# Optimization experiments

Hardware: AMD Instinct MI355X
Metric: run time of the kernel (lower is better)

## Reference

```python
import jax, jax.numpy as jnp
import numpy as np

N = 50000        # num_nodes
D = 512          # input_dim == output_dim (residual update requires equality)
EU = 100000      # undirected edges; directed E = 2*EU = 200000
STEP = 0.5       # step_size


def setup_inputs() -> dict:
    key = jax.random.key(0)
    ks = jax.random.split(key, 5)
    x = jax.random.normal(ks[0], (N, D), jnp.float32)
    # symmetric edge list without self loops: store (s,d) then (d,s)
    src = jax.random.randint(ks[1], (EU,), 0, N, dtype=jnp.int32)
    off = jax.random.randint(ks[2], (EU,), 1, N, dtype=jnp.int32)
    dst = (src + off) % N
    edge_index = jnp.stack([jnp.concatenate([src, dst]),
                            jnp.concatenate([dst, src])])  # [2, 2*EU]
    # reverse-edge index: edge e < EU reverses to e+EU and vice versa
    ar = jnp.arange(EU, dtype=jnp.int32)
    right_idx = jnp.concatenate([ar + EU, ar])
    # params: nn.Linear(D, D) and sheaf_learner nn.Linear(2D, 1, bias=False)
    W_lin = jax.random.normal(ks[3], (D, D), jnp.float32) / np.sqrt(D)
    b_lin = jnp.zeros((D,), jnp.float32)
    w_sheaf = jax.random.normal(ks[4], (2 * D,), jnp.float32) / np.sqrt(2 * D)
    return {"x": x, "W_lin": W_lin, "b_lin": b_lin, "w_sheaf": w_sheaf,
            "edge_index": edge_index, "right_idx": right_idx}


def reference(x, W_lin, b_lin, w_sheaf, edge_index, right_idx):
    row, col = edge_index[0], edge_index[1]
    d = x.shape[1]
    # sheaf_learner(cat([x_row, x_col])) == (x @ w[:d])[row] + (x @ w[d:])[col]
    s = x @ w_sheaf[:d]                      # [N]
    t = x @ w_sheaf[d:]                      # [N]
    maps = jnp.tanh(s[row] + t[col])         # [E] scalar restriction maps
    # off-diagonal Laplacian values: -F_e(row) * F_reverse(e)
    non_diag = -maps * maps[right_idx]       # [E]
    diag_maps = jax.ops.segment_sum(maps ** 2, row, num_segments=N)  # [N]
    d_inv = (diag_maps + 1.0) ** -0.5        # [N]
    norm_maps = d_inv[row] * non_diag * d_inv[col]                   # [E]
    diag = d_inv * diag_maps * d_inv                                 # [N]
    # y = linear(x); L @ y done as diag term + edge scatter
    y = x @ W_lin.T + b_lin                  # [N, D]
    Ly = diag[:, None] * y + jax.ops.segment_sum(
        norm_maps[:, None] * y[col], row, num_segments=N)
    return x - STEP * Ly
```

## Files before the change

### kernel.cpp

```cpp
#include <hip/hip_runtime.h>
#include <hip/hip_bf16.h>
#include <cstdint>
#include <cstddef>


#define DD 512
#define STEPSZ 0.5f
#define SLOTS 32

typedef __bf16 bf16;
typedef __bf16 bf16x8 __attribute__((ext_vector_type(8)));
typedef __bf16 bf16x4 __attribute__((ext_vector_type(4)));
typedef float f32x4 __attribute__((ext_vector_type(4)));

#define GLOAD16(g, l)                                                     \
  __builtin_amdgcn_global_load_lds(                                       \
      (const __attribute__((address_space(1))) void*)(g),                 \
      (__attribute__((address_space(3))) void*)(l), 16, 0, 0)

__global__ __launch_bounds__(256) void k_prep(
    const float* __restrict__ x, const float* __restrict__ wsheaf,
    const float* __restrict__ wlin, bf16* __restrict__ xbf,
    bf16* __restrict__ wbf, float* __restrict__ s, float* __restrict__ t,
    float* __restrict__ dmaps, int* __restrict__ fill, int n) {
  if (blockIdx.x < 256) {
    int i = (blockIdx.x * 256 + threadIdx.x) * 4;
    float4 v = *(const float4*)(wlin + i);
    bf16x4 p;
    p[0] = (bf16)v.x; p[1] = (bf16)v.y; p[2] = (bf16)v.z; p[3] = (bf16)v.w;
    *(bf16x4*)(wbf + i) = p;
    int zi = blockIdx.x * 256 + threadIdx.x;
    if (zi < n) { dmaps[zi] = 0.0f; fill[zi] = 0; }
    return;
  }
  int lane = threadIdx.x & 63;
  int row = ((blockIdx.x - 256) << 2) + (threadIdx.x >> 6);
  if (row >= n) return;
  const float* xr = x + (size_t)row * DD + lane * 8;
  float4 a = *(const float4*)xr;
  float4 b = *(const float4*)(xr + 4);
  bf16x8 p;
  p[0] = (bf16)a.x; p[1] = (bf16)a.y; p[2] = (bf16)a.z; p[3] = (bf16)a.w;
  p[4] = (bf16)b.x; p[5] = (bf16)b.y; p[6] = (bf16)b.z; p[7] = (bf16)b.w;
  *(bf16x8*)(xbf + (size_t)row * DD + lane * 8) = p;
  const float* w1 = wsheaf + lane * 8;
  const float* w2 = wsheaf + DD + lane * 8;
  float4 wa = *(const float4*)w1, wb = *(const float4*)(w1 + 4);
  float4 wc = *(const float4*)w2, wd = *(const float4*)(w2 + 4);
  float sv = a.x * wa.x + a.y * wa.y + a.z * wa.z + a.w * wa.w +
             b.x * wb.x + b.y * wb.y + b.z * wb.z + b.w * wb.w;
  float tv = a.x * wc.x + a.y * wc.y + a.z * wc.z + a.w * wc.w +
             b.x * wd.x + b.y * wd.y + b.z * wd.z + b.w * wd.w;
  #pragma unroll
  for (int o = 32; o > 0; o >>= 1) {
    sv += __shfl_xor(sv, o);
    tv += __shfl_xor(tv, o);
  }
  if (lane == 0) { s[row] = sv; t[row] = tv; }
}

__global__ __launch_bounds__(256) void k_fill(
    const int* __restrict__ ei, const float* __restrict__ s,
    const float* __restrict__ t, float* __restrict__ dmaps,
    int* __restrict__ fill, int* __restrict__ ccol, float* __restrict__ cval,
    int E) {
  int e = blockIdx.x * 256 + threadIdx.x;
  if (e >= E) return;
  int r = ei[e], c = ei[E + e];
  float sr = s[r], tc = t[c], sc = s[c], tr = t[r];
  float me = tanhf(sr + tc);
  float mr = tanhf(sc + tr);
  atomicAdd(dmaps + r, me * me);
  int p = atomicAdd(fill + r, 1);
  if (p < SLOTS) {
    ccol[(size_t)r * SLOTS + p] = c;
    cval[(size_t)r * SLOTS + p] = -me * mr;
  }
}

__global__ __launch_bounds__(256) void k_gather(
    const bf16* __restrict__ xb, const float* __restrict__ dmaps,
    const int* __restrict__ fill, const int* __restrict__ ccol,
    const float* __restrict__ cval, bf16* __restrict__ u,
    float* __restrict__ cb, int n) {
  int lane = threadIdx.x & 63;
  int row = (blockIdx.x << 2) + (threadIdx.x >> 6);
  if (row >= n) return;
  int c0 = lane * 8;
  float dm = dmaps[row];
  float inv_r = rsqrtf(dm + 1.0f);
  float dg = dm / (dm + 1.0f);
  bf16x8 xv = *(const bf16x8*)(xb + (size_t)row * DD + c0);
  float acc[8];
  #pragma unroll
  for (int j = 0; j < 8; ++j) acc[j] = dg * (float)xv[j];
  int cnt = fill[row];
  if (cnt > SLOTS) cnt = SLOTS;
  const int* cc = ccol + (size_t)row * SLOTS;
  const float* cv = cval + (size_t)row * SLOTS;
  unsigned nm1 = (unsigned)(n - 1);
  float cbs = 0.0f;
  for (int i = 0; i < cnt; i += 4) {
    int4 c4 = *(const int4*)(cc + i);
    float4 v4 = *(const float4*)(cv + i);
    int rem = cnt - i;
    unsigned ca = min((unsigned)c4.x, nm1);
    unsigned cbi = min((unsigned)c4.y, nm1);
    unsigned cg = min((unsigned)c4.z, nm1);
    unsigned cd = min((unsigned)c4.w, nm1);
    bf16x8 na = *(const bf16x8*)(xb + (size_t)ca * DD + c0);
    bf16x8 nb = *(const bf16x8*)(xb + (size_t)cbi * DD + c0);
    bf16x8 ng = *(const bf16x8*)(xb + (size_t)cg * DD + c0);
    bf16x8 nd = *(const bf16x8*)(xb + (size_t)cd * DD + c0);
    float va = rem > 0 ? v4.x * inv_r * rsqrtf(dmaps[ca] + 1.0f) : 0.0f;
    float vb = rem > 1 ? v4.y * inv_r * rsqrtf(dmaps[cbi] + 1.0f) : 0.0f;
    float vg = rem > 2 ? v4.z * inv_r * rsqrtf(dmaps[cg] + 1.0f) : 0.0f;
    float vd = rem > 3 ? v4.w * inv_r * rsqrtf(dmaps[cd] + 1.0f) : 0.0f;
    cbs += va + vb + vg + vd;
    #pragma unroll
    for (int j = 0; j < 8; ++j)
      acc[j] += va * (float)na[j] + vb * (float)nb[j] + vg * (float)ng[j] +
                vd * (float)nd[j];
  }
  bf16x8 o;
  #pragma unroll
  for (int j = 0; j < 8; ++j) o[j] = (bf16)acc[j];
  *(bf16x8*)(u + (size_t)row * DD + c0) = o;
  if (lane == 0) cb[row] = dg + cbs;
}

__global__ __launch_bounds__(256, 4) void k_gemm(
    const bf16* __restrict__ ub, const bf16* __restrict__ wbf,
    const float* __restrict__ bias, const float* __restrict__ x,
    const bf16* __restrict__ xb, const float* __restrict__ cb,
    float* __restrict__ out, int M, int nwg, int use_bf) {
  __shared__ __align__(16) char smem[36864];
  bf16* lds = (bf16*)smem;
  int orig = blockIdx.x;
  int q = nwg >> 3, r = nwg & 7;
  int xcd = orig & 7;
  int wgid = (xcd < r ? xcd * (q + 1) : r * (q + 1) + (xcd - r) * q) +
             (orig >> 3);
  int bm = wgid >> 2, bn = wgid & 3;
  int tid = threadIdx.x, w = tid >> 6, lane = tid & 63;
  int wr = w >> 1, wc = w & 1;
  int lhi = lane >> 4;

  int row_local = lane >> 2;
  int kc = (lane & 3) ^ (row_local & 3);
  const bf16* gA[2];
  const bf16* gB[2];
  bf16* lA[2];
  bf16* lB[2];
  #pragma unroll
  for (int c = 0; c < 2; ++c) {
    int rloc = c * 64 + w * 16 + row_local;
    int ga = bm * 128 + rloc;
    if (ga > M - 1) ga = M - 1;
    gA[c] = ub + (size_t)ga * DD + kc * 8;
    gB[c] = wbf + (size_t)(bn * 128 + rloc) * DD + kc * 8;
    lA[c] = lds + (c * 64 + w * 16) * 32;
    lB[c] = lds + 4096 + (c * 64 + w * 16) * 32;
  }

  f32x4 acc[4][4] = {};
  int arow = (wr * 64 + (lane & 15)) * 32;
  int brow = (wc * 64 + (lane & 15)) * 32;
  int sl = ((lhi ^ (lane & 3))) * 8;

  #pragma unroll
  for (int c = 0; c < 2; ++c) {
    GLOAD16(gA[c], lA[c]);
    GLOAD16(gB[c], lB[c]);
  }
  __syncthreads();

  #pragma unroll
  for (int t = 0; t < 16; ++t) {
    int cbuf = (t & 1) * 8192;
    if (t + 1 < 16) {
      int nbuf = ((t + 1) & 1) * 8192;
      int k0 = (t + 1) * 32;
      #pragma unroll
      for (int c = 0; c < 2; ++c) {
        GLOAD16(gA[c] + k0, lA[c] + nbuf);
        GLOAD16(gB[c] + k0, lB[c] + nbuf);
      }
    }
    const bf16* base = lds + cbuf;
    bf16x8 af[4], bfr[4];
    #pragma unroll
    for (int m = 0; m < 4; ++m)
      af[m] = *(const bf16x8*)(base + arow + m * 512 + sl);
    #pragma unroll
    for (int nn = 0; nn < 4; ++nn)
      bfr[nn] = *(const bf16x8*)(base + 4096 + brow + nn * 512 + sl);
    #pragma unroll
    for (int m = 0; m < 4; ++m)
      #pragma unroll
      for (int nn = 0; nn < 4; ++nn)
        acc[m][nn] = __builtin_amdgcn_mfma_f32_16x16x32_bf16(
            af[m], bfr[nn], acc[m][nn], 0, 0, 0);
    __syncthreads();
  }

  int rowbase = bm * 128 + wr * 64;
  int clamped = rowbase + lane;
  if (clamped > M - 1) clamped = M - 1;
  float cbl = cb[clamped];
  float* ltile = (float*)smem + w * 2304;
  int prow = lane >> 3;
  int pc4 = lane & 7;
  #pragma unroll
  for (int h = 0; h < 2; ++h) {
    #pragma unroll
    for (int m = 0; m < 4; ++m)
      #pragma unroll
      for (int n2 = 0; n2 < 2; ++n2)
        #pragma unroll
        for (int rr = 0; rr < 4; ++rr) {
          int row = m * 16 + lhi * 4 + rr;
          ltile[row * 36 + n2 * 16 + (lane & 15)] = acc[m][h * 2 + n2][rr];
        }
    int gcol = bn * 128 + wc * 64 + h * 32 + pc4 * 4;
    float4 bb = *(const float4*)(bias + gcol);
    #pragma unroll
    for (int p = 0; p < 8; ++p) {
      int row = p * 8 + prow;
      int gr = rowbase + row;
      float cbr = __shfl(cbl, row);
      if (gr < M) {
        float4 v = *(const float4*)(ltile + row * 36 + pc4 * 4);
        float xr0, xr1, xr2, xr3;
        if (use_bf) {
          bf16x4 xv = *(const bf16x4*)(xb + (size_t)gr * DD + gcol);
          xr0 = (float)xv[0]; xr1 = (float)xv[1];
          xr2 = (float)xv[2]; xr3 = (float)xv[3];
        } else {
          float4 xv = *(const float4*)(x + (size_t)gr * DD + gcol);
          xr0 = xv.x; xr1 = xv.y; xr2 = xv.z; xr3 = xv.w;
        }
        float4 o;
        o.x = xr0 - STEPSZ * (v.x + cbr * bb.x);
        o.y = xr1 - STEPSZ * (v.y + cbr * bb.y);
        o.z = xr2 - STEPSZ * (v.z + cbr * bb.z);
        o.w = xr3 - STEPSZ * (v.w + cbr * bb.w);
        *(float4*)(out + (size_t)gr * DD + gcol) = o;
      }
    }
  }
}

extern "C" void kernel_launch(void* const* d_in, const int* in_sizes, int n_in,
                              void* d_out, int out_size, void* d_ws,
                              size_t ws_size, hipStream_t stream) {
  const float* x = (const float*)d_in[0];
  const float* W = (const float*)d_in[1];
  const float* b = (const float*)d_in[2];
  const float* wsheaf = (const float*)d_in[3];
  const int* ei = (const int*)d_in[4];
  const int* right = (const int*)d_in[5];
  (void)right;
  int N = in_sizes[0] / DD;
  int E = in_sizes[5];

  char* ws = (char*)d_ws;
  size_t p = 0;
  auto alloc = [&](size_t bytes) -> char* {
    char* r = ws + p;
    p += (bytes + 255) & ~(size_t)255;
    return r;
  };
  bf16* ub = (bf16*)alloc((size_t)N * DD * 2);
  float* cval = (float*)alloc((size_t)N * SLOTS * 4);
  int* ccol = (int*)alloc((size_t)N * SLOTS * 4);
  float* s = (float*)alloc((size_t)N * 4);
  float* t = (float*)alloc((size_t)N * 4);
  float* cb = (float*)alloc((size_t)N * 4);
  bf16* wbf = (bf16*)alloc((size_t)DD * DD * 2);
  char* zblock = alloc((size_t)N * 8);
  float* diag_maps = (float*)zblock;
  int* fill = (int*)(zblock + (size_t)N * 4);

  size_t xbf_bytes = (size_t)N * DD * 2;
  int use_bf = (p + xbf_bytes) <= ws_size;
  bf16* xbf = use_bf ? (bf16*)alloc(xbf_bytes) : (bf16*)d_out;

  k_prep<<<256 + (N + 3) / 4, 256, 0, stream>>>(x, wsheaf, W, xbf, wbf, s, t,
                                                diag_maps, fill, N);
  k_fill<<<(E + 255) / 256, 256, 0, stream>>>(ei, s, t, diag_maps, fill, ccol,
                                              cval, E);
  k_gather<<<(N + 3) / 4, 256, 0, stream>>>(xbf, diag_maps, fill, ccol, cval,
                                            ub, cb, N);
  int MT = (N + 127) / 128;
  int nwg = MT * 4;
  k_gemm<<<nwg, 256, 0, stream>>>(ub, wbf, b, x, xbf, cb, (float*)d_out, N,
                                  nwg, use_bf);
}
```

Before: 158.5 us.

## Load GEMM MFMA operands directly from global memory instead of LDS staging

The GEMM mainloop no longer stages A and B tiles through double-buffered LDS with global_load_lds and per-step barriers. Each lane now reads its bf16x8 fragments straight from global memory and relies on the cache for reuse across waves. This removes LDS traffic and the per-iteration __syncthreads, but each tile element is fetched from cache by several waves and the loads are less coalesced (16-byte strided rows).

New measurement: 227.8 us. 1.44x slower.

```diff
diff --git a/kernel.cpp b/kernel.cpp
--- a/kernel.cpp
+++ b/kernel.cpp
@@ -12,11 +12,6 @@
 typedef __bf16 bf16x8 __attribute__((ext_vector_type(8)));
 typedef __bf16 bf16x4 __attribute__((ext_vector_type(4)));
 typedef float f32x4 __attribute__((ext_vector_type(4)));
-
-#define GLOAD16(g, l)                                                     \
-  __builtin_amdgcn_global_load_lds(                                       \
-      (const __attribute__((address_space(1))) void*)(g),                 \
-      (__attribute__((address_space(3))) void*)(l), 16, 0, 0)
 
 __global__ __launch_bounds__(256) void k_prep(
     const float* __restrict__ x, const float* __restrict__ wsheaf,
@@ -134,8 +129,7 @@
     const float* __restrict__ bias, const float* __restrict__ x,
     const bf16* __restrict__ xb, const float* __restrict__ cb,
     float* __restrict__ out, int M, int nwg, int use_bf) {
-  __shared__ __align__(16) char smem[36864];
-  bf16* lds = (bf16*)smem;
+  __shared__ __align__(16) float smem[9216];
   int orig = blockIdx.x;
   int q = nwg >> 3, r = nwg & 7;
   int xcd = orig & 7;
@@ -146,69 +140,38 @@
   int wr = w >> 1, wc = w & 1;
   int lhi = lane >> 4;
 
-  int row_local = lane >> 2;
-  int kc = (lane & 3) ^ (row_local & 3);
-  const bf16* gA[2];
-  const bf16* gB[2];
-  bf16* lA[2];
-  bf16* lB[2];
-  #pragma unroll
-  for (int c = 0; c < 2; ++c) {
-    int rloc = c * 64 + w * 16 + row_local;
-    int ga = bm * 128 + rloc;
+  const bf16* pA[4];
+  const bf16* pB[4];
+  #pragma unroll
+  for (int m = 0; m < 4; ++m) {
+    int ga = bm * 128 + wr * 64 + m * 16 + (lane & 15);
     if (ga > M - 1) ga = M - 1;
-    gA[c] = ub + (size_t)ga * DD + kc * 8;
-    gB[c] = wbf + (size_t)(bn * 128 + rloc) * DD + kc * 8;
-    lA[c] = lds + (c * 64 + w * 16) * 32;
-    lB[c] = lds + 4096 + (c * 64 + w * 16) * 32;
+    pA[m] = ub + (size_t)ga * DD + lhi * 8;
+    int gb = bn * 128 + wc * 64 + m * 16 + (lane & 15);
+    pB[m] = wbf + (size_t)gb * DD + lhi * 8;
   }
 
   f32x4 acc[4][4] = {};
-  int arow = (wr * 64 + (lane & 15)) * 32;
-  int brow = (wc * 64 + (lane & 15)) * 32;
-  int sl = ((lhi ^ (lane & 3))) * 8;
-
-  #pragma unroll
-  for (int c = 0; c < 2; ++c) {
-    GLOAD16(gA[c], lA[c]);
-    GLOAD16(gB[c], lB[c]);
-  }
-  __syncthreads();
-
-  #pragma unroll
-  for (int t = 0; t < 16; ++t) {
-    int cbuf = (t & 1) * 8192;
-    if (t + 1 < 16) {
-      int nbuf = ((t + 1) & 1) * 8192;
-      int k0 = (t + 1) * 32;
-      #pragma unroll
-      for (int c = 0; c < 2; ++c) {
-        GLOAD16(gA[c] + k0, lA[c] + nbuf);
-        GLOAD16(gB[c] + k0, lB[c] + nbuf);
-      }
-    }
-    const bf16* base = lds + cbuf;
+  #pragma unroll
+  for (int s = 0; s < 16; ++s) {
     bf16x8 af[4], bfr[4];
     #pragma unroll
-    for (int m = 0; m < 4; ++m)
-      af[m] = *(const bf16x8*)(base + arow + m * 512 + sl);
-    #pragma unroll
-    for (int nn = 0; nn < 4; ++nn)
-      bfr[nn] = *(const bf16x8*)(base + 4096 + brow + nn * 512 + sl);
+    for (int m = 0; m < 4; ++m) af[m] = *(const bf16x8*)(pA[m] + s * 32);
+    #pragma unroll
+    for (int nn = 0; nn < 4; ++nn) bfr[nn] = *(const bf16x8*)(pB[nn] + s * 32);
     #pragma unroll
     for (int m = 0; m < 4; ++m)
       #pragma unroll
       for (int nn = 0; nn < 4; ++nn)
         acc[m][nn] = __builtin_amdgcn_mfma_f32_16x16x32_bf16(
             af[m], bfr[nn], acc[m][nn], 0, 0, 0);
-    __syncthreads();
   }
 
   int rowbase = bm * 128 + wr * 64;
   int clamped = rowbase + lane;
   if (clamped > M - 1) clamped = M - 1;
   float cbl = cb[clamped];
-  float* ltile = (float*)smem + w * 2304;
+  float* ltile = smem + w * 2304;
   int prow = lane >> 3;
   int pc4 = lane & 7;
   #pragma unroll
```
